# Kernel tuning notes

Measured on AMD Instinct MI355X. Metric: run time of the kernel, lower is better.

## Reference

```python
import jax, jax.numpy as jnp
import numpy as np

BN_EPS = 1e-5

def _conv1x1(x, w, b):
    # x: [B,C,H,W], w: [O,C], b: [O]
    return jnp.einsum('bchw,oc->bohw', x, w) + b[None, :, None, None]

def _maxpool2x2(x):
    B, C, H, W = x.shape
    return x.reshape(B, C, H // 2, 2, W // 2, 2).max(axis=(3, 5))

def setup_inputs() -> dict:
    key = jax.random.key(0)
    ks = jax.random.split(key, 6)
    B, C, H, W = 8, 256, 64, 64
    Ci = C // 2  # inter_channels default
    x = jax.random.normal(ks[0], (B, C, H, W), jnp.float32)
    s = lambda k, sh: jax.random.normal(k, sh, jnp.float32) * 0.02
    return {
        'x': x,
        'w_g': s(ks[1], (Ci, C)), 'b_g': jnp.zeros((Ci,), jnp.float32),
        'w_theta': s(ks[2], (Ci, C)), 'b_theta': jnp.zeros((Ci,), jnp.float32),
        'w_phi': s(ks[3], (Ci, C)), 'b_phi': jnp.zeros((Ci,), jnp.float32),
        'w_w': s(ks[4], (C, Ci)), 'b_w': jnp.zeros((C,), jnp.float32),
        'bn_gamma': 1.0 + 0.1 * jax.random.normal(ks[5], (C,), jnp.float32),
        'bn_beta': jnp.zeros((C,), jnp.float32),
    }

def reference(x, w_g, b_g, w_theta, b_theta, w_phi, b_phi, w_w, b_w, bn_gamma, bn_beta):
    B, C, H, W = x.shape
    Ci = w_g.shape[0]
    # projections (sub_sample=True: maxpool 2x2 on g and phi)
    g_x = _maxpool2x2(_conv1x1(x, w_g, b_g)).reshape(B, Ci, -1)          # [B,Ci,M]
    g_x = g_x.transpose(0, 2, 1)                                          # [B,M,Ci]
    theta_x = _conv1x1(x, w_theta, b_theta).reshape(B, Ci, -1)            # [B,Ci,N]
    theta_x = theta_x.transpose(0, 2, 1)                                  # [B,N,Ci]
    phi_x = _maxpool2x2(_conv1x1(x, w_phi, b_phi)).reshape(B, Ci, -1)     # [B,Ci,M]
    # unscaled embedded-Gaussian attention (no 1/sqrt(d), as in source)
    f = jnp.einsum('bnc,bcm->bnm', theta_x, phi_x)                        # [B,N,M]
    f_div_C = jax.nn.softmax(f, axis=-1)
    y = jnp.einsum('bnm,bmc->bnc', f_div_C, g_x)                          # [B,N,Ci]
    y = y.transpose(0, 2, 1).reshape(B, Ci, H, W)
    # W: 1x1 conv + BatchNorm (training mode: batch statistics)
    wy = _conv1x1(y, w_w, b_w)                                            # [B,C,H,W]
    mean = wy.mean(axis=(0, 2, 3), keepdims=True)
    var = wy.var(axis=(0, 2, 3), keepdims=True)
    wy = (wy - mean) * jax.lax.rsqrt(var + BN_EPS)
    wy = wy * bn_gamma[None, :, None, None] + bn_beta[None, :, None, None]
    return wy + x
```

## Files before the change

### kernel.cpp

```cpp
#include <hip/hip_runtime.h>
#include <hip/hip_bf16.h>

#define NB 8
#define NC 256
#define NCI 128
#define NSP 4096
#define NM 1024

typedef float f32x4 __attribute__((ext_vector_type(4)));
typedef float f32x16 __attribute__((ext_vector_type(16)));
typedef short s16x8 __attribute__((ext_vector_type(8)));
typedef unsigned short u16;

#define OFF_XH  (0ull)
#define OFF_XL  (16777216ull)
#define OFF_THT (33554432ull)
#define OFF_PHT (41943040ull)
#define OFF_GP  (44040192ull)
#define OFF_YH  (46137344ull)
#define OFF_YL  (54525952ull)
#define OFF_WY  (0ull)
#define OFF_WBH (62914560ull)
#define OFF_WBL (63111168ull)
#define OFF_WWH (63307776ull)
#define OFF_WWL (63373312ull)
#define OFF_S   (63438848ull)

#define GLL(src, dst) __builtin_amdgcn_global_load_lds( \
    (const __attribute__((address_space(1))) unsigned*)(src), \
    (__attribute__((address_space(3))) unsigned*)(dst), 16, 0, 0)

__device__ __forceinline__ u16 f2bf(float f) {
  union { __hip_bfloat16 h; u16 u; } v;
  v.h = __float2bfloat16(f);
  return v.u;
}
__device__ __forceinline__ float bf2f(u16 u) {
  union { unsigned u; float f; } v;
  v.u = (unsigned)u << 16;
  return v.f;
}
__device__ __forceinline__ u16 bfmax4(u16 a, u16 b, u16 c, u16 d) {
  float v = fmaxf(fmaxf(bf2f(a), bf2f(b)), fmaxf(bf2f(c), bf2f(d)));
  return f2bf(v);
}
__device__ __forceinline__ unsigned cvtpk(float lo, float hi) {
  unsigned r;
  asm volatile("v_cvt_pk_bf16_f32 %0, %1, %2" : "=v"(r) : "v"(lo), "v"(hi));
  return r;
}

__global__ void zero_stats(float* s) { s[threadIdx.x] = 0.f; }

__global__ __launch_bounds__(256) void wcvt(
    const float* __restrict__ wg, const float* __restrict__ wth,
    const float* __restrict__ wph, const float* __restrict__ ww,
    u16* __restrict__ wbh, u16* __restrict__ wbl,
    u16* __restrict__ wwh, u16* __restrict__ wwl)
{
  int idx = blockIdx.x * 256 + threadIdx.x;
  if (idx < 384 * 256) {
    int row = idx >> 8, k = idx & 255;
    float v = row < 128 ? wg[row * 256 + k]
            : row < 256 ? wth[(row - 128) * 256 + k]
                        : wph[(row - 256) * 256 + k];
    u16 h = f2bf(v);
    wbh[idx] = h;
    wbl[idx] = f2bf(v - bf2f(h));
  } else {
    int j = idx - 384 * 256;
    float v = ww[j];
    u16 h = f2bf(v);
    wwh[j] = h;
    wwl[j] = f2bf(v - bf2f(h));
  }
}

__global__ __launch_bounds__(256) void xt_cvt(const float* __restrict__ x,
                                              u16* __restrict__ xh, u16* __restrict__ xl)
{
  __shared__ float t[64 * 68];
  const int n0 = blockIdx.x << 6, c0 = blockIdx.y << 6, b = blockIdx.z;
  const int tid = threadIdx.x;
  const int cl = tid >> 4, n4 = (tid & 15) << 2;
#pragma unroll
  for (int it = 0; it < 4; ++it) {
    int c = it * 16 + cl;
    float4 v = *(const float4*)&x[((size_t)(b * NC + c0 + c)) * NSP + n0 + n4];
    *(float4*)&t[c * 68 + n4] = v;
  }
  __syncthreads();
#pragma unroll
  for (int it = 0; it < 2; ++it) {
    int task = it * 256 + tid;
    int n = task >> 3, cc = (task & 7) << 3;
    u16 oh[8], ol[8];
#pragma unroll
    for (int i = 0; i < 8; ++i) {
      float v = t[(cc + i) * 68 + n];
      oh[i] = f2bf(v);
      ol[i] = f2bf(v - bf2f(oh[i]));
    }
    size_t dst = ((size_t)(b * NSP + n0 + n)) * NC + c0 + cc;
    *(s16x8*)&xh[dst] = *(s16x8*)oh;
    *(s16x8*)&xl[dst] = *(s16x8*)ol;
  }
}

__global__ __launch_bounds__(512, 1) void proj_fused(
    const u16* __restrict__ xh, const u16* __restrict__ xl,
    const u16* __restrict__ wbh, const u16* __restrict__ wbl,
    const float* __restrict__ bg, const float* __restrict__ bth,
    const float* __restrict__ bph,
    u16* __restrict__ thT, u16* __restrict__ phT, u16* __restrict__ gp)
{
  __shared__ char smem[132608];
  u16* xsh = (u16*)smem;
  u16* xsl = (u16*)(smem + 16384);
  u16* wsh = (u16*)(smem + 32768);
  u16* wsl = (u16*)(smem + 81920);
  u16* outl = (u16*)smem;
  float* bias = (float*)(smem + 131072);

  const int b = blockIdx.y, h2 = blockIdx.x;
  const int n0 = h2 << 7;
  const int tid = threadIdx.x;
  const int wave = tid >> 6, lane = tid & 63;
  const int lo16 = lane & 15, hi4 = lane >> 4;
  const int wr = wave >> 1, wc = wave & 1;
  const int obase = wr * 96, nbase = wc * 64;

  if (tid < 384)
    bias[tid] = tid < 128 ? bg[tid] : tid < 256 ? bth[tid - 128] : bph[tid - 256];

  f32x4 acc[6][4];
#pragma unroll
  for (int i = 0; i < 6; ++i)
#pragma unroll
    for (int j = 0; j < 4; ++j) acc[i][j] = (f32x4){0.f, 0.f, 0.f, 0.f};

  for (int step = 0; step < 4; ++step) {
    __syncthreads();
#pragma unroll
    for (int i = 0; i < 2; ++i) {
      int ci = i * 512 + tid;
      int n = ci >> 3, slot = ci & 7;
      size_t rowb = ((size_t)(b * NSP + n0 + n)) * 512 + step * 128 + ((slot ^ (n & 7)) << 4);
      GLL((const char*)xh + rowb, (char*)xsh + (size_t)(i * 512 + (tid & ~63)) * 16);
      GLL((const char*)xl + rowb, (char*)xsl + (size_t)(i * 512 + (tid & ~63)) * 16);
    }
#pragma unroll
    for (int i = 0; i < 6; ++i) {
      int ci = i * 512 + tid;
      int o = ci >> 3, slot = ci & 7;
      size_t rowb = (size_t)o * 512 + step * 128 + ((slot ^ (o & 7)) << 4);
      GLL((const char*)wbh + rowb, (char*)wsh + (size_t)(i * 512 + (tid & ~63)) * 16);
      GLL((const char*)wbl + rowb, (char*)wsl + (size_t)(i * 512 + (tid & ~63)) * 16);
    }
    __syncthreads();

#pragma unroll
    for (int kc = 0; kc < 2; ++kc) {
      const int sl = kc * 4 + hi4;
      s16x8 bfh[4], bfl[4];
#pragma unroll
      for (int fn = 0; fn < 4; ++fn) {
        int n = nbase + fn * 16 + lo16;
        int off = (int)n * 128 + ((sl ^ (n & 7)) << 4);
        bfh[fn] = *(const s16x8*)((const char*)xsh + off);
        bfl[fn] = *(const s16x8*)((const char*)xsl + off);
      }
      __builtin_amdgcn_s_setprio(1);
#pragma unroll
      for (int fo = 0; fo < 6; ++fo) {
        int o = obase + fo * 16 + lo16;
        int off = (int)o * 128 + ((sl ^ (o & 7)) << 4);
        s16x8 afh = *(const s16x8*)((const char*)wsh + off);
        s16x8 afl = *(const s16x8*)((const char*)wsl + off);
#pragma unroll
        for (int fn = 0; fn < 4; ++fn) {
          acc[fo][fn] = __builtin_amdgcn_mfma_f32_16x16x32_bf16(afh, bfh[fn], acc[fo][fn], 0, 0, 0);
          acc[fo][fn] = __builtin_amdgcn_mfma_f32_16x16x32_bf16(afh, bfl[fn], acc[fo][fn], 0, 0, 0);
          acc[fo][fn] = __builtin_amdgcn_mfma_f32_16x16x32_bf16(afl, bfh[fn], acc[fo][fn], 0, 0, 0);
        }
      }
      __builtin_amdgcn_s_setprio(0);
    }
  }

  __syncthreads();
#pragma unroll
  for (int fo = 0; fo < 6; ++fo) {
    int orow = obase + fo * 16 + hi4 * 4;
    f32x4 bv = *(const f32x4*)&bias[orow];
#pragma unroll
    for (int fn = 0; fn < 4; ++fn) {
      int n = nbase + fn * 16 + lo16;
#pragma unroll
      for (int r = 0; r < 4; ++r)
        outl[(orow + r) * 137 + n] = f2bf(acc[fo][fn][r] + bv[r]);
    }
  }
  __syncthreads();

#pragma unroll
  for (int it = 0; it < 4; ++it) {
    int task = it * 512 + tid;
    int n = task >> 4, cc = (task & 15) << 3;
    u16 o[8];
#pragma unroll
    for (int i = 0; i < 8; ++i) o[i] = outl[(128 + cc + i) * 137 + n];
    *(s16x8*)&thT[((size_t)(b * NSP + n0 + n)) * NCI + cc] = *(s16x8*)o;
  }
  {
    int c = tid >> 2, wq = tid & 3;
    u16 o[8];
#pragma unroll
    for (int j = 0; j < 8; ++j) {
      int w2 = wq * 8 + j;
      o[j] = bfmax4(outl[c * 137 + 2 * w2], outl[c * 137 + 2 * w2 + 1],
                    outl[c * 137 + 64 + 2 * w2], outl[c * 137 + 64 + 2 * w2 + 1]);
    }
    *(s16x8*)&gp[((size_t)(b * NCI + c)) * NM + (h2 << 5) + wq * 8] = *(s16x8*)o;
  }
  {
    int w2 = tid >> 4, cc = (tid & 15) << 3;
    u16 o[8];
#pragma unroll
    for (int i = 0; i < 8; ++i) {
      int c = 256 + cc + i;
      o[i] = bfmax4(outl[c * 137 + 2 * w2], outl[c * 137 + 2 * w2 + 1],
                    outl[c * 137 + 64 + 2 * w2], outl[c * 137 + 64 + 2 * w2 + 1]);
    }
    *(s16x8*)&phT[((size_t)(b * NM + (h2 << 5) + w2)) * NCI + cc] = *(s16x8*)o;
  }
}

__global__ __launch_bounds__(256, 1) void attn_mfma(
    const u16* __restrict__ thT, const u16* __restrict__ phT,
    const u16* __restrict__ gP, u16* __restrict__ yh, u16* __restrict__ yl)
{
  __shared__ char smem[65536];

  const int b = blockIdx.y;
  const int n0 = blockIdx.x << 7;
  const int tid = threadIdx.x;
  const int wave = tid >> 6;
  const int lane = tid & 63;
  const int l31 = lane & 31;
  const int hi1 = lane >> 5;
  const int qbase = n0 + (wave << 5);
  const int swl = (l31 & 7) << 4;

  s16x8 thb[8];
  {
    const u16* tr = &thT[((size_t)b * NSP + qbase + l31) * NCI + hi1 * 8];
#pragma unroll
    for (int kc = 0; kc < 8; ++kc) thb[kc] = *(const s16x8*)&tr[kc * 16];
  }

  f32x16 yacc[4];
#pragma unroll
  for (int ct = 0; ct < 4; ++ct) yacc[ct] = (f32x16)0.f;
  float m_i = -3e38f, l_i = 0.f;

  auto stage = [&](int s, int m0) {
    char* pdst = smem + s * 16384;
    char* gdst = smem + 32768 + s * 16384;
#pragma unroll
    for (int i = 0; i < 4; ++i) {
      int ci = i * 256 + tid;
      int m = ci >> 4, cb = (ci & 15) << 4;
      const char* src = (const char*)phT + (((size_t)b * NM + m0 + m) << 8) + (cb ^ ((m & 7) << 4));
      GLL(src, pdst + (size_t)(i * 256 + (tid & ~63)) * 16);
    }
#pragma unroll
    for (int i = 0; i < 4; ++i) {
      int ci = i * 256 + tid;
      int c = ci >> 3, mb = (ci & 7) << 4;
      const char* src = (const char*)gP + (((size_t)b * NCI + c) << 11) + m0 * 2 + (mb ^ ((c & 7) << 4));
      GLL(src, gdst + (size_t)(i * 256 + (tid & ~63)) * 16);
    }
  };

  stage(0, 0);
  __syncthreads();
  int cur = 0;

  for (int mt = 0; mt < 16; ++mt) {
    if (mt < 15) stage(cur ^ 1, (mt + 1) << 6);
    const char* ph = smem + cur * 16384;
    const char* gg = smem + 32768 + cur * 16384;

    f32x16 s0 = (f32x16)0.f, s1 = (f32x16)0.f;
    __builtin_amdgcn_s_setprio(1);
#pragma unroll
    for (int kc = 0; kc < 8; ++kc) {
      int cofs = (kc * 32 + hi1 * 16);
      s16x8 a0 = *(const s16x8*)(ph + l31 * 256 + (cofs ^ swl));
      s16x8 a1 = *(const s16x8*)(ph + (32 + l31) * 256 + (cofs ^ swl));
      s0 = __builtin_amdgcn_mfma_f32_32x32x16_bf16(a0, thb[kc], s0, 0, 0, 0);
      s1 = __builtin_amdgcn_mfma_f32_32x32x16_bf16(a1, thb[kc], s1, 0, 0, 0);
    }
    __builtin_amdgcn_s_setprio(0);

    float pm = s0[0];
#pragma unroll
    for (int i = 1; i < 16; ++i) pm = fmaxf(pm, s0[i]);
#pragma unroll
    for (int i = 0; i < 16; ++i) pm = fmaxf(pm, s1[i]);
    pm = fmaxf(pm, __shfl_xor(pm, 32));
    float mn = fmaxf(m_i, pm);
    float sc = __expf(m_i - mn);
    float rs = 0.f;
#pragma unroll
    for (int i = 0; i < 16; ++i) { s0[i] = __expf(s0[i] - mn); rs += s0[i]; }
#pragma unroll
    for (int i = 0; i < 16; ++i) { s1[i] = __expf(s1[i] - mn); rs += s1[i]; }
    rs += __shfl_xor(rs, 32);
    l_i = l_i * sc + rs;
    m_i = mn;
#pragma unroll
    for (int ct = 0; ct < 4; ++ct)
#pragma unroll
      for (int i = 0; i < 16; ++i) yacc[ct][i] *= sc;

    s16x8 pb[4];
#pragma unroll
    for (int km = 0; km < 4; ++km) {
      int r0 = (km & 1) * 8;
      unsigned X0, X1, X2, X3;
      if (km < 2) {
        X0 = cvtpk(s0[r0 + 0], s0[r0 + 1]);
        X1 = cvtpk(s0[r0 + 2], s0[r0 + 3]);
        X2 = cvtpk(s0[r0 + 4], s0[r0 + 5]);
        X3 = cvtpk(s0[r0 + 6], s0[r0 + 7]);
      } else {
        X0 = cvtpk(s1[r0 + 0], s1[r0 + 1]);
        X1 = cvtpk(s1[r0 + 2], s1[r0 + 3]);
        X2 = cvtpk(s1[r0 + 4], s1[r0 + 5]);
        X3 = cvtpk(s1[r0 + 6], s1[r0 + 7]);
      }
      asm volatile("v_permlane32_swap_b32 %0, %1" : "+v"(X0), "+v"(X2));
      asm volatile("v_permlane32_swap_b32 %0, %1" : "+v"(X1), "+v"(X3));
      unsigned d[4] = {X0, X1, X2, X3};
      pb[km] = *(s16x8*)d;
    }

    __builtin_amdgcn_s_setprio(1);
#pragma unroll
    for (int ct = 0; ct < 4; ++ct) {
      const char* grow = gg + (ct * 32 + l31) * 128;
#pragma unroll
      for (int km = 0; km < 4; ++km) {
        s16x8 ga = *(const s16x8*)(grow + ((km * 32 + hi1 * 16) ^ swl));
        yacc[ct] = __builtin_amdgcn_mfma_f32_32x32x16_bf16(ga, pb[km], yacc[ct], 0, 0, 0);
      }
    }
    __builtin_amdgcn_s_setprio(0);

    __syncthreads();
    cur ^= 1;
  }

  float inv = 1.f / l_i;
#pragma unroll
  for (int ct = 0; ct < 4; ++ct)
#pragma unroll
    for (int i = 0; i < 16; ++i) yacc[ct][i] *= inv;

  u16* bounce = (u16*)smem;
  const int qq = lane >> 1, c0 = (lane & 1) << 6;
#pragma unroll
  for (int pass = 0; pass < 2; ++pass) {
    __syncthreads();
#pragma unroll
    for (int ct = 0; ct < 4; ++ct) {
#pragma unroll
      for (int rp = 0; rp < 8; ++rp) {
        int r = rp * 2;
        int c = ct * 32 + (r & 3) + 8 * (r >> 2) + 4 * hi1;
        float v0 = yacc[ct][r], v1 = yacc[ct][r + 1];
        u16 h0 = f2bf(v0), h1 = f2bf(v1);
        u16 w0 = h0, w1 = h1;
        if (pass) { w0 = f2bf(v0 - bf2f(h0)); w1 = f2bf(v1 - bf2f(h1)); }
        *(unsigned*)&bounce[wave * 4224 + l31 * 132 + c] = (unsigned)w0 | ((unsigned)w1 << 16);
      }
    }
    __syncthreads();
    u16* dst = pass ? yl : yh;
    size_t row = ((size_t)b * NSP + qbase + qq) * NCI + c0;
#pragma unroll
    for (int k = 0; k < 8; ++k)
      *(s16x8*)&dst[row + k * 8] = *(const s16x8*)&bounce[wave * 4224 + qq * 132 + c0 + k * 8];
  }
}

__global__ __launch_bounds__(512, 1) void conv_w_mfma(
    const u16* __restrict__ yh, const u16* __restrict__ yl,
    const u16* __restrict__ wwh, const u16* __restrict__ wwl,
    const float* __restrict__ bw, float* __restrict__ wy,
    float* __restrict__ s1g, float* __restrict__ s2g)
{
  __shared__ char smem[102400];
  u16* wsh = (u16*)smem;
  u16* wsl = (u16*)(smem + 32768);
  u16* ysh = (u16*)(smem + 65536);
  u16* ysl = (u16*)(smem + 81920);
  float (*sums1)[256] = (float(*)[256])(smem + 98304);
  float (*sums2)[256] = (float(*)[256])(smem + 100352);

  const int b = blockIdx.y, n0 = blockIdx.x << 7;
  const int tid = threadIdx.x;
  const int wave = tid >> 6, lane = tid & 63;
  const int lo16 = lane & 15, hi4 = lane >> 4;
  const int wr = wave >> 1, wc = wave & 1;
  const int obase = wr * 64, nbase = wc * 64;

  f32x4 acc[4][4];
#pragma unroll
  for (int i = 0; i < 4; ++i)
#pragma unroll
    for (int j = 0; j < 4; ++j) acc[i][j] = (f32x4){0.f, 0.f, 0.f, 0.f};

  for (int step = 0; step < 2; ++step) {
    __syncthreads();
#pragma unroll
    for (int i = 0; i < 4; ++i) {
      int ci = i * 512 + tid;
      int o = ci >> 3, slot = ci & 7;
      size_t rowb = (size_t)o * 256 + step * 128 + ((slot ^ (o & 7)) << 4);
      GLL((const char*)wwh + rowb, (char*)wsh + (size_t)(i * 512 + (tid & ~63)) * 16);
      GLL((const char*)wwl + rowb, (char*)wsl + (size_t)(i * 512 + (tid & ~63)) * 16);
    }
#pragma unroll
    for (int i = 0; i < 2; ++i) {
      int ci = i * 512 + tid;
      int n = ci >> 3, slot = ci & 7;
      size_t rowb = ((size_t)(b * NSP + n0 + n)) * 256 + step * 128 + ((slot ^ (n & 7)) << 4);
      GLL((const char*)yh + rowb, (char*)ysh + (size_t)(i * 512 + (tid & ~63)) * 16);
      GLL((const char*)yl + rowb, (char*)ysl + (size_t)(i * 512 + (tid & ~63)) * 16);
    }
    __syncthreads();

#pragma unroll
    for (int kc = 0; kc < 2; ++kc) {
      const int sl = kc * 4 + hi4;
      s16x8 bfh[4], bfl[4];
#pragma unroll
      for (int fn = 0; fn < 4; ++fn) {
        int n = nbase + fn * 16 + lo16;
        int off = (int)n * 128 + ((sl ^ (n & 7)) << 4);
        bfh[fn] = *(const s16x8*)((const char*)ysh + off);
        bfl[fn] = *(const s16x8*)((const char*)ysl + off);
      }
      __builtin_amdgcn_s_setprio(1);
#pragma unroll
      for (int fo = 0; fo < 4; ++fo) {
        int o = obase + fo * 16 + lo16;
        int off = (int)o * 128 + ((sl ^ (o & 7)) << 4);
        s16x8 afh = *(const s16x8*)((const char*)wsh + off);
        s16x8 afl = *(const s16x8*)((const char*)wsl + off);
#pragma unroll
        for (int fn = 0; fn < 4; ++fn) {
          acc[fo][fn] = __builtin_amdgcn_mfma_f32_16x16x32_bf16(afh, bfh[fn], acc[fo][fn], 0, 0, 0);
          acc[fo][fn] = __builtin_amdgcn_mfma_f32_16x16x32_bf16(afh, bfl[fn], acc[fo][fn], 0, 0, 0);
          acc[fo][fn] = __builtin_amdgcn_mfma_f32_16x16x32_bf16(afl, bfh[fn], acc[fo][fn], 0, 0, 0);
        }
      }
      __builtin_amdgcn_s_setprio(0);
    }
  }

#pragma unroll
  for (int fo = 0; fo < 4; ++fo) {
    int orow = obase + fo * 16 + hi4 * 4;
    float bv[4];
#pragma unroll
    for (int r = 0; r < 4; ++r) bv[r] = bw[orow + r];
    float ss[4] = {0.f, 0.f, 0.f, 0.f}, sq[4] = {0.f, 0.f, 0.f, 0.f};
#pragma unroll
    for (int fn = 0; fn < 4; ++fn) {
      int col = n0 + nbase + fn * 16 + lo16;
#pragma unroll
      for (int r = 0; r < 4; ++r) {
        float v = acc[fo][fn][r] + bv[r];
        wy[((size_t)(b * NC) + orow + r) * NSP + col] = v;
        ss[r] += v;
        sq[r] += v * v;
      }
    }
#pragma unroll
    for (int r = 0; r < 4; ++r) {
#pragma unroll
      for (int d = 1; d < 16; d <<= 1) {
        ss[r] += __shfl_xor(ss[r], d);
        sq[r] += __shfl_xor(sq[r], d);
      }
    }
    if (lo16 == 0) {
#pragma unroll
      for (int r = 0; r < 4; ++r) {
        sums1[wc][orow + r] = ss[r];
        sums2[wc][orow + r] = sq[r];
      }
    }
  }
  __syncthreads();
  if (tid < 256) {
    atomicAdd(&s1g[tid], sums1[0][tid] + sums1[1][tid]);
    atomicAdd(&s2g[tid], sums2[0][tid] + sums2[1][tid]);
  }
}

__global__ __launch_bounds__(256) void bn_res4(
    const float* __restrict__ wy, const float* __restrict__ x,
    const float* __restrict__ s1, const float* __restrict__ s2,
    const float* __restrict__ gamma, const float* __restrict__ beta,
    float* __restrict__ out)
{
  int i4 = (blockIdx.x * 256 + threadIdx.x) << 2;
  int c = (i4 >> 12) & 255;
  const float cnt = 1.f / 32768.f;
  float mean = s1[c] * cnt;
  float var = s2[c] * cnt - mean * mean;
  float inv = rsqrtf(var + 1e-5f) * gamma[c];
  float bet = beta[c];
  float4 w = *(const float4*)&wy[i4];
  float4 xv = *(const float4*)&x[i4];
  float4 o;
  o.x = (w.x - mean) * inv + bet + xv.x;
  o.y = (w.y - mean) * inv + bet + xv.y;
  o.z = (w.z - mean) * inv + bet + xv.z;
  o.w = (w.w - mean) * inv + bet + xv.w;
  *(float4*)&out[i4] = o;
}

extern "C" void kernel_launch(void* const* d_in, const int* in_sizes, int n_in,
                              void* d_out, int out_size, void* d_ws, size_t ws_size,
                              hipStream_t stream) {
  const float* x    = (const float*)d_in[0];
  const float* w_g  = (const float*)d_in[1];
  const float* b_g  = (const float*)d_in[2];
  const float* w_th = (const float*)d_in[3];
  const float* b_th = (const float*)d_in[4];
  const float* w_ph = (const float*)d_in[5];
  const float* b_ph = (const float*)d_in[6];
  const float* w_w  = (const float*)d_in[7];
  const float* b_w  = (const float*)d_in[8];
  const float* gam  = (const float*)d_in[9];
  const float* bet  = (const float*)d_in[10];
  float* out = (float*)d_out;
  char* ws = (char*)d_ws;

  u16*   xh  = (u16*)(ws + OFF_XH);
  u16*   xl  = (u16*)(ws + OFF_XL);
  u16*   thT = (u16*)(ws + OFF_THT);
  u16*   phT = (u16*)(ws + OFF_PHT);
  u16*   gp  = (u16*)(ws + OFF_GP);
  u16*   yhb = (u16*)(ws + OFF_YH);
  u16*   ylb = (u16*)(ws + OFF_YL);
  float* wy  = (float*)(ws + OFF_WY);
  u16*   wbh = (u16*)(ws + OFF_WBH);
  u16*   wbl = (u16*)(ws + OFF_WBL);
  u16*   wwh = (u16*)(ws + OFF_WWH);
  u16*   wwl = (u16*)(ws + OFF_WWL);
  float* s1  = (float*)(ws + OFF_S);
  float* s2  = s1 + 256;

  wcvt<<<dim3(512), 256, 0, stream>>>(w_g, w_th, w_ph, w_w, wbh, wbl, wwh, wwl);
  zero_stats<<<dim3(1), 512, 0, stream>>>(s1);
  xt_cvt<<<dim3(64, 4, 8), 256, 0, stream>>>(x, xh, xl);

  proj_fused<<<dim3(32, 8), 512, 0, stream>>>(xh, xl, wbh, wbl, b_g, b_th, b_ph, thT, phT, gp);

  attn_mfma<<<dim3(32, 8), 256, 0, stream>>>(thT, phT, gp, yhb, ylb);

  conv_w_mfma<<<dim3(32, 8), 512, 0, stream>>>(yhb, ylb, wwh, wwl, b_w, wy, s1, s2);

  bn_res4<<<dim3(8192), 256, 0, stream>>>(wy, x, s1, s2, gam, bet, out);
}
```

Before: 119.6 us.

## Split attention key range across two wave groups and merge softmax states

The attention kernel now launches 512 threads per block, with two groups of four waves each covering half of the 1024 keys (split-K flash attention). The second group writes its partial accumulators and running max/sum to LDS, and the first group merges them with rescaling before the bf16 hi/lo output. The aim is more waves per CU to hide latency, since only 256 blocks run on the GPU. The cost is 128KB of LDS per block, extra LDS traffic for the merge, and a staging loop that is now doubled in size.

```diff
diff --git a/kernel.cpp b/kernel.cpp
--- a/kernel.cpp
+++ b/kernel.cpp
@@ -236,20 +236,22 @@
   }
 }
 
-__global__ __launch_bounds__(256, 1) void attn_mfma(
+__global__ __launch_bounds__(512, 2) void attn_mfma(
     const u16* __restrict__ thT, const u16* __restrict__ phT,
     const u16* __restrict__ gP, u16* __restrict__ yh, u16* __restrict__ yl)
 {
-  __shared__ char smem[65536];
+  __shared__ char smem[131072];
 
   const int b = blockIdx.y;
   const int n0 = blockIdx.x << 7;
   const int tid = threadIdx.x;
   const int wave = tid >> 6;
+  const int qg = wave & 3;
+  const int kh = wave >> 2;
   const int lane = tid & 63;
   const int l31 = lane & 31;
   const int hi1 = lane >> 5;
-  const int qbase = n0 + (wave << 5);
+  const int qbase = n0 + (qg << 5);
   const int swl = (l31 & 7) << 4;
 
   s16x8 thb[8];
@@ -264,22 +266,25 @@
   for (int ct = 0; ct < 4; ++ct) yacc[ct] = (f32x16)0.f;
   float m_i = -3e38f, l_i = 0.f;
 
-  auto stage = [&](int s, int m0) {
-    char* pdst = smem + s * 16384;
-    char* gdst = smem + 32768 + s * 16384;
-#pragma unroll
-    for (int i = 0; i < 4; ++i) {
-      int ci = i * 256 + tid;
-      int m = ci >> 4, cb = (ci & 15) << 4;
-      const char* src = (const char*)phT + (((size_t)b * NM + m0 + m) << 8) + (cb ^ ((m & 7) << 4));
-      GLL(src, pdst + (size_t)(i * 256 + (tid & ~63)) * 16);
-    }
-#pragma unroll
-    for (int i = 0; i < 4; ++i) {
-      int ci = i * 256 + tid;
-      int c = ci >> 3, mb = (ci & 7) << 4;
-      const char* src = (const char*)gP + (((size_t)b * NCI + c) << 11) + m0 * 2 + (mb ^ ((c & 7) << 4));
-      GLL(src, gdst + (size_t)(i * 256 + (tid & ~63)) * 16);
+  auto stage = [&](int s, int step) {
+    char* base = smem + s * 65536;
+    const int m0a = step << 6, m0b = (step + 8) << 6;
+#pragma unroll
+    for (int it = 0; it < 8; ++it) {
+      const int rg = it >> 1;
+      int r = ((it & 1) << 9) + tid;
+      char* dst = base + rg * 16384 + (size_t)(((it & 1) << 9) + (tid & ~63)) * 16;
+      if (rg == 0 || rg == 2) {
+        int m0 = (rg == 0) ? m0a : m0b;
+        int m = r >> 4, cb = (r & 15) << 4;
+        const char* src = (const char*)phT + (((size_t)b * NM + m0 + m) << 8) + (cb ^ ((m & 7) << 4));
+        GLL(src, dst);
+      } else {
+        int m0 = (rg == 1) ? m0a : m0b;
+        int c = r >> 3, mb = (r & 7) << 4;
+        const char* src = (const char*)gP + (((size_t)b * NCI + c) << 11) + m0 * 2 + (mb ^ ((c & 7) << 4));
+        GLL(src, dst);
+      }
     }
   };
 
@@ -287,10 +292,10 @@
   __syncthreads();
   int cur = 0;
 
-  for (int mt = 0; mt < 16; ++mt) {
-    if (mt < 15) stage(cur ^ 1, (mt + 1) << 6);
-    const char* ph = smem + cur * 16384;
-    const char* gg = smem + 32768 + cur * 16384;
+  for (int step = 0; step < 8; ++step) {
+    if (step < 7) stage(cur ^ 1, step + 1);
+    const char* ph = smem + cur * 65536 + kh * 32768;
+    const char* gg = ph + 16384;
 
     f32x16 s0 = (f32x16)0.f, s1 = (f32x16)0.f;
     __builtin_amdgcn_s_setprio(1);
@@ -363,17 +368,43 @@
     cur ^= 1;
   }
 
-  float inv = 1.f / l_i;
+  float* yx = (float*)smem;
+  float* ml = (float*)(smem + 65536);
+  const int slot = (qg << 6) + lane;
+  if (kh == 1) {
+#pragma unroll
+    for (int ct = 0; ct < 4; ++ct)
+#pragma unroll
+      for (int i4 = 0; i4 < 4; ++i4) {
+        f32x4 v = {yacc[ct][i4 * 4 + 0], yacc[ct][i4 * 4 + 1],
+                   yacc[ct][i4 * 4 + 2], yacc[ct][i4 * 4 + 3]};
+        *(f32x4*)((char*)yx + (size_t)(((ct * 4 + i4) << 8) + slot) * 16) = v;
+      }
+    ml[slot * 2] = m_i;
+    ml[slot * 2 + 1] = l_i;
+  }
+  __syncthreads();
+  if (kh == 1) return;
+
+  float m1 = ml[slot * 2], l1 = ml[slot * 2 + 1];
+  float mm = fmaxf(m_i, m1);
+  float sc0 = __expf(m_i - mm), sc1 = __expf(m1 - mm);
+  float inv = 1.f / (l_i * sc0 + l1 * sc1);
+  float a0 = sc0 * inv, a1 = sc1 * inv;
 #pragma unroll
   for (int ct = 0; ct < 4; ++ct)
 #pragma unroll
-    for (int i = 0; i < 16; ++i) yacc[ct][i] *= inv;
-
-  u16* bounce = (u16*)smem;
+    for (int i4 = 0; i4 < 4; ++i4) {
+      f32x4 v = *(const f32x4*)((const char*)yx + (size_t)(((ct * 4 + i4) << 8) + slot) * 16);
+#pragma unroll
+      for (int j = 0; j < 4; ++j)
+        yacc[ct][i4 * 4 + j] = yacc[ct][i4 * 4 + j] * a0 + v[j] * a1;
+    }
+
+  u16* bounce = (u16*)(smem + 67584) + qg * 4224;
   const int qq = lane >> 1, c0 = (lane & 1) << 6;
 #pragma unroll
   for (int pass = 0; pass < 2; ++pass) {
-    __syncthreads();
 #pragma unroll
     for (int ct = 0; ct < 4; ++ct) {
 #pragma unroll
@@ -384,15 +415,16 @@
         u16 h0 = f2bf(v0), h1 = f2bf(v1);
         u16 w0 = h0, w1 = h1;
         if (pass) { w0 = f2bf(v0 - bf2f(h0)); w1 = f2bf(v1 - bf2f(h1)); }
-        *(unsigned*)&bounce[wave * 4224 + l31 * 132 + c] = (unsigned)w0 | ((unsigned)w1 << 16);
-      }
-    }
-    __syncthreads();
+        *(unsigned*)&bounce[l31 * 132 + c] = (unsigned)w0 | ((unsigned)w1 << 16);
+      }
+    }
+    asm volatile("s_waitcnt lgkmcnt(0)" ::: "memory");
     u16* dst = pass ? yl : yh;
     size_t row = ((size_t)b * NSP + qbase + qq) * NCI + c0;
 #pragma unroll
     for (int k = 0; k < 8; ++k)
-      *(s16x8*)&dst[row + k * 8] = *(const s16x8*)&bounce[wave * 4224 + qq * 132 + c0 + k * 8];
+      *(s16x8*)&dst[row + k * 8] = *(const s16x8*)&bounce[qq * 132 + c0 + k * 8];
+    asm volatile("s_waitcnt lgkmcnt(0)" ::: "memory");
   }
 }
 
@@ -574,7 +606,7 @@
 
   proj_fused<<<dim3(32, 8), 512, 0, stream>>>(xh, xl, wbh, wbl, b_g, b_th, b_ph, thT, phT, gp);
 
-  attn_mfma<<<dim3(32, 8), 256, 0, stream>>>(thT, phT, gp, yhb, ylb);
+  attn_mfma<<<dim3(32, 8), 512, 0, stream>>>(thT, phT, gp, yhb, ylb);
 
   conv_w_mfma<<<dim3(32, 8), 512, 0, stream>>>(yhb, ylb, wwh, wwl, b_w, wy, s1, s2);
 
```

Result: faster. 112.0 us (-6.3%).
